# Kernel tuning notes

Hardware: AMD Instinct MI355X
Metric: run time of the kernel (lower is better)

Reference implementation:

```python
import jax, jax.numpy as jnp
import numpy as np

B, T, D = 2, 2048, 1024
N, H = 16, 64  # num_heads, head_dim
LOG2E = 1.442695041
NEG_INF = -1.0e9


def setup_inputs() -> dict:
    key = jax.random.key(0)
    ks = jax.random.split(key, 6)
    return {
        "input_tensor": jax.random.normal(ks[0], (B, T, D), dtype=jnp.float32),
        "attention_mask": jax.random.randint(ks[1], (B, 1, T, T), 0, 2, dtype=jnp.int32),
        "wq": jax.random.normal(ks[2], (D, N, H), dtype=jnp.float32),
        "bq": jnp.zeros((N, H), dtype=jnp.float32),
        "wk": jax.random.normal(ks[3], (D, N, H), dtype=jnp.float32),
        "bk": jnp.zeros((N, H), dtype=jnp.float32),
        "wv": jax.random.normal(ks[4], (D, N, H), dtype=jnp.float32),
        "bv": jnp.zeros((N, H), dtype=jnp.float32),
        "wo": jax.random.normal(ks[5], (D, N, H), dtype=jnp.float32),
        "bo": jnp.zeros((D,), dtype=jnp.float32),
        "per_dim_scale": jnp.zeros((H,), dtype=jnp.float32),
    }


def reference(input_tensor, attention_mask, wq, bq, wk, bk, wv, bv, wo, bo, per_dim_scale):
    # QKV projections: [B,T,D] x [D,N,H] -> [B,T,N,H]
    q = jnp.einsum('btd,dnh->btnh', input_tensor, wq) + bq
    k = jnp.einsum('btd,dnh->btnh', input_tensor, wk) + bk
    v = jnp.einsum('btd,dnh->btnh', input_tensor, wv) + bv
    # per-dim query scaling: (log2(e)/sqrt(H)) * softplus(per_dim_scale)
    scale = (LOG2E / jnp.sqrt(jnp.asarray(H, q.dtype))) * jax.nn.softplus(per_dim_scale)
    q = q * scale
    # scores: [B,N,T,S]
    scores = jnp.einsum('btnh,bsnh->bnts', q, k)
    scores = jnp.where(attention_mask == 0, jnp.asarray(NEG_INF, scores.dtype), scores)
    weights = jax.nn.softmax(scores, axis=-1)
    # AV: [B,N,T,S] x [B,S,N,H] -> [B,T,N,H]
    attn_out = jnp.einsum('bnts,bsnh->btnh', weights, v)
    # output projection: [B,T,N,H] x [D,N,H] -> [B,T,D]
    return jnp.einsum('btnh,dnh->btd', attn_out, wo) + bo
```

## Files before the change

### kernel.cpp

```cpp
#include <hip/hip_runtime.h>
#include <math.h>

typedef __bf16 bf16;
typedef __attribute__((ext_vector_type(8))) __bf16 bf16x8;
typedef __attribute__((ext_vector_type(4))) __bf16 bf16x4;
typedef __attribute__((ext_vector_type(4))) float f32x4;

#define BB 2
#define TT 2048
#define DD 1024
#define NHD 16
#define HD 64
#define MM (BB*TT)
#define LOG2E_F 1.442695041f
#define NEGINF_F (-1.0e9f)

__device__ __forceinline__ void gld16(const bf16* g, bf16* l)
{
    __builtin_amdgcn_global_load_lds(
        (const __attribute__((address_space(1))) unsigned int*)g,
        (__attribute__((address_space(3))) unsigned int*)l, 16, 0, 0);
}

__global__ __launch_bounds__(256)
void prep_all(const float* __restrict__ X, const int* __restrict__ m,
              const float* __restrict__ wq, const float* __restrict__ wk,
              const float* __restrict__ wv, const float* __restrict__ wo,
              bf16* __restrict__ Xh, bf16* __restrict__ Xl,
              bf16* __restrict__ qkh, bf16* __restrict__ qkl,
              bf16* __restrict__ vh, bf16* __restrict__ ob,
              unsigned* __restrict__ bits)
{
    __shared__ float tile[32][33];
    const int bid = blockIdx.x;
    const int t   = threadIdx.x;

    if (bid < 4096) {
        int i = bid * 256 + t;
        float4 v = ((const float4*)X)[i];
        float f[4] = {v.x, v.y, v.z, v.w};
        bf16x4 h, l;
        #pragma unroll
        for (int j = 0; j < 4; ++j) {
            bf16 hh = (bf16)f[j];
            h[j] = hh;
            l[j] = (bf16)(f[j] - (float)hh);
        }
        *(bf16x4*)(Xh + (size_t)i * 4) = h;
        *(bf16x4*)(Xl + (size_t)i * 4) = l;
        return;
    }
    if (bid < 8192) {
        const int idx = bid - 4096;
        const int z   = idx >> 10;
        const int bx  = (idx & 31) << 5;
        const int by  = ((idx >> 5) & 31) << 5;
        const int r   = t >> 3;
        const int c4  = (t & 7) << 2;
        if (z == 3) {
            float4 v = *(const float4*)(wo + (size_t)(by + r) * 1024 + bx + c4);
            bf16x4 o = { (bf16)v.x, (bf16)v.y, (bf16)v.z, (bf16)v.w };
            *(bf16x4*)(ob + (size_t)(by + r) * 1024 + bx + c4) = o;
            return;
        }
        const float* src = (z == 0) ? wq : ((z == 1) ? wk : wv);
        bf16* oh = (z == 0) ? qkh : ((z == 1) ? qkh + 1048576 : vh);
        bf16* ol = (z == 0) ? qkl : ((z == 1) ? qkl + 1048576 : nullptr);
        float4 v = *(const float4*)(src + (size_t)(by + r) * 1024 + bx + c4);
        tile[r][c4+0] = v.x; tile[r][c4+1] = v.y;
        tile[r][c4+2] = v.z; tile[r][c4+3] = v.w;
        __syncthreads();
        bf16x4 hv, lv;
        #pragma unroll
        for (int j = 0; j < 4; ++j) {
            float f = tile[c4 + j][r];
            bf16 h = (bf16)f;
            hv[j] = h;
            lv[j] = (bf16)(f - (float)h);
        }
        *(bf16x4*)(oh + (size_t)(bx + r) * 1024 + by + c4) = hv;
        if (ol)
            *(bf16x4*)(ol + (size_t)(bx + r) * 1024 + by + c4) = lv;
        return;
    }
    {
        int i = (bid - 8192) * 256 + t;
        int lane = t & 63;
        int v = m[i];
        unsigned long long bl = __ballot(v != 0);
        if ((lane & 31) == 0)
            bits[i >> 5] = (unsigned)(bl >> (lane & 32));
    }
}

__global__ __launch_bounds__(256)
void gemm_proj(const bf16* __restrict__ Xh, const bf16* __restrict__ Xl,
               const bf16* __restrict__ Wh, const bf16* __restrict__ Wl,
               const bf16* __restrict__ Wvh,
               const float* __restrict__ bq, const float* __restrict__ bk,
               const float* __restrict__ bv, const float* __restrict__ pds,
               bf16* __restrict__ oQh, bf16* __restrict__ oQl,
               bf16* __restrict__ oKh, bf16* __restrict__ oKl,
               bf16* __restrict__ oVt)
{
    __shared__ bf16 S[4][128 * 32];

    const int bid  = blockIdx.x;
    const int t    = threadIdx.x;
    const int lane = t & 63;
    const int w    = t >> 6;
    const int quad = lane >> 4, l15 = lane & 15;
    const int wm   = (w >> 1) << 6;
    const int wn   = (w & 1)  << 6;

    const int jr0 = ((w * 2 + 0) << 4) + (lane >> 2);
    const int jr1 = ((w * 2 + 1) << 4) + (lane >> 2);
    const int kch = (lane & 3) << 3;
    const int off0 = (w * 2 + 0) * 512;
    const int off1 = (w * 2 + 1) * 512;

    if (bid < 512) {
        const int m0 = (bid >> 4) << 7;
        const int n0 = (bid & 15) << 7;
        bf16* Ah = S[0]; bf16* Al = S[1]; bf16* Bh = S[2]; bf16* Bl = S[3];

        const bf16* pAh0 = Xh + (size_t)(m0 + jr0) * DD + kch;
        const bf16* pAh1 = Xh + (size_t)(m0 + jr1) * DD + kch;
        const bf16* pAl0 = Xl + (size_t)(m0 + jr0) * DD + kch;
        const bf16* pAl1 = Xl + (size_t)(m0 + jr1) * DD + kch;
        const bf16* pBh0 = Wh + (size_t)(n0 + jr0) * DD + kch;
        const bf16* pBh1 = Wh + (size_t)(n0 + jr1) * DD + kch;
        const bf16* pBl0 = Wl + (size_t)(n0 + jr0) * DD + kch;
        const bf16* pBl1 = Wl + (size_t)(n0 + jr1) * DD + kch;

        f32x4 acc[4][4] = {};

        for (int k0 = 0; k0 < DD; k0 += 32) {
            __syncthreads();
            gld16(pAh0 + k0, Ah + off0);  gld16(pAh1 + k0, Ah + off1);
            gld16(pAl0 + k0, Al + off0);  gld16(pAl1 + k0, Al + off1);
            gld16(pBh0 + k0, Bh + off0);  gld16(pBh1 + k0, Bh + off1);
            gld16(pBl0 + k0, Bl + off0);  gld16(pBl1 + k0, Bl + off1);
            __syncthreads();

            bf16x8 ah[4], bh[4];
            #pragma unroll
            for (int mt = 0; mt < 4; ++mt)
                ah[mt] = *(const bf16x8*)(Ah + (wm + (mt << 4) + l15) * 32 + (quad << 3));
            #pragma unroll
            for (int nt = 0; nt < 4; ++nt)
                bh[nt] = *(const bf16x8*)(Bh + (wn + (nt << 4) + l15) * 32 + (quad << 3));
            #pragma unroll
            for (int mt = 0; mt < 4; ++mt)
                #pragma unroll
                for (int nt = 0; nt < 4; ++nt)
                    acc[mt][nt] = __builtin_amdgcn_mfma_f32_16x16x32_bf16(
                        ah[mt], bh[nt], acc[mt][nt], 0, 0, 0);

            bf16x8 bl[4];
            #pragma unroll
            for (int nt = 0; nt < 4; ++nt)
                bl[nt] = *(const bf16x8*)(Bl + (wn + (nt << 4) + l15) * 32 + (quad << 3));
            #pragma unroll
            for (int mt = 0; mt < 4; ++mt)
                #pragma unroll
                for (int nt = 0; nt < 4; ++nt)
                    acc[mt][nt] = __builtin_amdgcn_mfma_f32_16x16x32_bf16(
                        ah[mt], bl[nt], acc[mt][nt], 0, 0, 0);

            bf16x8 al[4];
            #pragma unroll
            for (int mt = 0; mt < 4; ++mt)
                al[mt] = *(const bf16x8*)(Al + (wm + (mt << 4) + l15) * 32 + (quad << 3));
            #pragma unroll
            for (int mt = 0; mt < 4; ++mt)
                #pragma unroll
                for (int nt = 0; nt < 4; ++nt)
                    acc[mt][nt] = __builtin_amdgcn_mfma_f32_16x16x32_bf16(
                        al[mt], bh[nt], acc[mt][nt], 0, 0, 0);
        }

        #pragma unroll
        for (int nt = 0; nt < 4; ++nt) {
            const int col = n0 + wn + (nt << 4) + l15;
            const int isQ = (col < 1024);
            const int nh  = col & 1023;
            const int n   = nh >> 6, h = nh & 63;
            const float bcol = isQ ? bq[nh] : bk[nh];
            float s = 1.f;
            if (isQ) {
                float x  = pds[h];
                float sp = fmaxf(x, 0.f) + log1pf(expf(-fabsf(x)));
                s = (LOG2E_F * LOG2E_F / 8.0f) * sp;
            }
            bf16* dH = isQ ? oQh : oKh;
            bf16* dL = isQ ? oQl : oKl;
            #pragma unroll
            for (int mt = 0; mt < 4; ++mt) {
                #pragma unroll
                for (int reg = 0; reg < 4; ++reg) {
                    const int row = m0 + wm + (mt << 4) + (quad << 2) + reg;
                    const int bi  = row >> 11;
                    const int tt  = row & (TT - 1);
                    float val = (acc[mt][nt][reg] + bcol) * s;
                    const size_t idx = (((size_t)bi * NHD + n) * TT + tt) * HD + h;
                    bf16 hi = (bf16)val;
                    dH[idx] = hi;
                    dL[idx] = (bf16)(val - (float)hi);
                }
            }
        }
    } else {
        const int idx = bid - 512;
        const int m0  = (idx >> 5) << 7;
        const int n0  = (idx & 31) << 7;
        bf16* As = S[0]; bf16* Bs = S[2];

        const bf16* Ap0 = Wvh + (size_t)(m0 + jr0) * DD + kch;
        const bf16* Ap1 = Wvh + (size_t)(m0 + jr1) * DD + kch;
        const bf16* Bp0 = Xh  + (size_t)(n0 + jr0) * DD + kch;
        const bf16* Bp1 = Xh  + (size_t)(n0 + jr1) * DD + kch;

        f32x4 acc[4][4] = {};

        for (int k0 = 0; k0 < DD; k0 += 32) {
            __syncthreads();
            gld16(Ap0 + k0, As + off0);
            gld16(Ap1 + k0, As + off1);
            gld16(Bp0 + k0, Bs + off0);
            gld16(Bp1 + k0, Bs + off1);
            __syncthreads();
            bf16x8 af[4], bfm[4];
            #pragma unroll
            for (int mt = 0; mt < 4; ++mt)
                af[mt] = *(const bf16x8*)(As + (wm + (mt << 4) + l15) * 32 + (quad << 3));
            #pragma unroll
            for (int nt = 0; nt < 4; ++nt)
                bfm[nt] = *(const bf16x8*)(Bs + (wn + (nt << 4) + l15) * 32 + (quad << 3));
            #pragma unroll
            for (int mt = 0; mt < 4; ++mt)
                #pragma unroll
                for (int nt = 0; nt < 4; ++nt)
                    acc[mt][nt] = __builtin_amdgcn_mfma_f32_16x16x32_bf16(
                        af[mt], bfm[nt], acc[mt][nt], 0, 0, 0);
        }

        #pragma unroll
        for (int nt = 0; nt < 4; ++nt) {
            const int col = n0 + wn + (nt << 4) + l15;
            const int bi  = col >> 11;
            const int tt  = col & (TT - 1);
            #pragma unroll
            for (int mt = 0; mt < 4; ++mt) {
                #pragma unroll
                for (int reg = 0; reg < 4; ++reg) {
                    const int row = m0 + wm + (mt << 4) + (quad << 2) + reg;
                    float val = acc[mt][nt][reg] + bv[row];
                    oVt[((size_t)bi * 1024 + row) * TT + tt] = (bf16)val;
                }
            }
        }
    }
}

__global__ __launch_bounds__(256)
void gemm_out(const bf16* __restrict__ A, const bf16* __restrict__ Bt,
              const float* __restrict__ bias, float* __restrict__ oF)
{
    __shared__ bf16 As[128 * 32];
    __shared__ bf16 Bs[128 * 32];

    const int t    = threadIdx.x;
    const int lane = t & 63;
    const int w    = t >> 6;
    const int quad = lane >> 4, l15 = lane & 15;
    const int m0   = blockIdx.y << 7;
    const int n0   = blockIdx.x << 7;
    const int wm   = (w >> 1) << 6;
    const int wn   = (w & 1)  << 6;

    const int jr0 = ((w * 2 + 0) << 4) + (lane >> 2);
    const int jr1 = ((w * 2 + 1) << 4) + (lane >> 2);
    const int kch = (lane & 3) << 3;

    bf16* lA0 = As + (w * 2 + 0) * 512;
    bf16* lA1 = As + (w * 2 + 1) * 512;
    bf16* lB0 = Bs + (w * 2 + 0) * 512;
    bf16* lB1 = Bs + (w * 2 + 1) * 512;

    const bf16* Ap0 = A  + (size_t)(m0 + jr0) * DD + kch;
    const bf16* Ap1 = A  + (size_t)(m0 + jr1) * DD + kch;
    const bf16* Bp0 = Bt + (size_t)(n0 + jr0) * DD + kch;
    const bf16* Bp1 = Bt + (size_t)(n0 + jr1) * DD + kch;

    f32x4 acc[4][4] = {};

    for (int k0 = 0; k0 < DD; k0 += 32) {
        __syncthreads();
        gld16(Ap0 + k0, lA0);
        gld16(Ap1 + k0, lA1);
        gld16(Bp0 + k0, lB0);
        gld16(Bp1 + k0, lB1);
        __syncthreads();
        bf16x8 af[4], bfm[4];
        #pragma unroll
        for (int mt = 0; mt < 4; ++mt)
            af[mt] = *(const bf16x8*)(As + (wm + (mt << 4) + l15) * 32 + (quad << 3));
        #pragma unroll
        for (int nt = 0; nt < 4; ++nt)
            bfm[nt] = *(const bf16x8*)(Bs + (wn + (nt << 4) + l15) * 32 + (quad << 3));
        #pragma unroll
        for (int mt = 0; mt < 4; ++mt)
            #pragma unroll
            for (int nt = 0; nt < 4; ++nt)
                acc[mt][nt] = __builtin_amdgcn_mfma_f32_16x16x32_bf16(
                    af[mt], bfm[nt], acc[mt][nt], 0, 0, 0);
    }

    #pragma unroll
    for (int nt = 0; nt < 4; ++nt) {
        const int col = n0 + wn + (nt << 4) + l15;
        const float bcol = bias[col];
        #pragma unroll
        for (int mt = 0; mt < 4; ++mt) {
            #pragma unroll
            for (int reg = 0; reg < 4; ++reg) {
                const int row = m0 + wm + (mt << 4) + (quad << 2) + reg;
                oF[(size_t)row * DD + col] = acc[mt][nt][reg] + bcol;
            }
        }
    }
}

__global__ __launch_bounds__(512)
void attn_mfma(const bf16* __restrict__ Qh, const bf16* __restrict__ Ql,
               const bf16* __restrict__ Kh, const bf16* __restrict__ Kl,
               const bf16* __restrict__ Vt, const unsigned* __restrict__ mbits,
               bf16* __restrict__ AO)
{
    __shared__ bf16 Ksh[64][72];
    __shared__ bf16 Ksl[64][72];
    __shared__ bf16 Vts[64][72];
    __shared__ bf16 Ps[8][16][72];
    __shared__ unsigned msk[128][2];

    const int t    = threadIdx.x;
    const int lane = t & 63;
    const int w    = t >> 6;
    const int quad = lane >> 4, l15 = lane & 15;
    const int bn   = blockIdx.y;
    const int b    = bn >> 4, n = bn & 15;
    const int q0   = blockIdx.x << 7;

    const bf16* Qbh = Qh + (size_t)bn * TT * HD;
    const bf16* Qbl = Ql + (size_t)bn * TT * HD;
    const bf16* Kbh = Kh + (size_t)bn * TT * HD;
    const bf16* Kbl = Kl + (size_t)bn * TT * HD;
    const bf16* Vtb = Vt + (size_t)bn * HD * TT;

    const int qrow = q0 + (w << 4) + l15;
    bf16x8 qfh[2], qfl[2];
    qfh[0] = *(const bf16x8*)(Qbh + (size_t)qrow * HD + (quad << 3));
    qfh[1] = *(const bf16x8*)(Qbh + (size_t)qrow * HD + 32 + (quad << 3));
    qfl[0] = *(const bf16x8*)(Qbl + (size_t)qrow * HD + (quad << 3));
    qfl[1] = *(const bf16x8*)(Qbl + (size_t)qrow * HD + 32 + (quad << 3));

    f32x4 O[4];
    #pragma unroll
    for (int i = 0; i < 4; ++i) O[i] = (f32x4){0.f,0.f,0.f,0.f};
    float m_i = -INFINITY;
    float l_i = 0.f;

    const int rS = t >> 3, cS = (t & 7) << 3;

    for (int kb = 0; kb < TT; kb += 64) {
        bf16x8 khv = *(const bf16x8*)(Kbh + (size_t)(kb + rS) * HD + cS);
        bf16x8 klv = *(const bf16x8*)(Kbl + (size_t)(kb + rS) * HD + cS);
        bf16x8 vv  = *(const bf16x8*)(Vtb + (size_t)rS * TT + kb + cS);
        unsigned mw = 0;
        if (t < 256)
            mw = mbits[((size_t)b * TT + q0 + (t >> 1)) * (TT / 32) + (kb >> 5) + (t & 1)];

        __syncthreads();
        *(bf16x8*)&Ksh[rS][cS] = khv;
        *(bf16x8*)&Ksl[rS][cS] = klv;
        *(bf16x8*)&Vts[rS][cS] = vv;
        if (t < 256) msk[t >> 1][t & 1] = mw;
        __syncthreads();

        f32x4 s_acc[4];
        #pragma unroll
        for (int i = 0; i < 4; ++i) s_acc[i] = (f32x4){0.f,0.f,0.f,0.f};
        #pragma unroll
        for (int k2 = 0; k2 < 2; ++k2) {
            #pragma unroll
            for (int nt = 0; nt < 4; ++nt) {
                bf16x8 bkh = *(const bf16x8*)&Ksh[(nt << 4) + l15][(k2 << 5) + (quad << 3)];
                bf16x8 bkl = *(const bf16x8*)&Ksl[(nt << 4) + l15][(k2 << 5) + (quad << 3)];
                s_acc[nt] = __builtin_amdgcn_mfma_f32_16x16x32_bf16(bkh, qfh[k2], s_acc[nt], 0, 0, 0);
                s_acc[nt] = __builtin_amdgcn_mfma_f32_16x16x32_bf16(bkl, qfh[k2], s_acc[nt], 0, 0, 0);
                s_acc[nt] = __builtin_amdgcn_mfma_f32_16x16x32_bf16(bkh, qfl[k2], s_acc[nt], 0, 0, 0);
            }
        }

        const unsigned w0 = msk[(w << 4) + l15][0];
        const unsigned w1 = msk[(w << 4) + l15][1];
        float sv[16];
        #pragma unroll
        for (int nt = 0; nt < 4; ++nt) {
            const unsigned word = (nt & 2) ? w1 : w0;
            #pragma unroll
            for (int reg = 0; reg < 4; ++reg) {
                const int bit = ((nt & 1) << 4) + (quad << 2) + reg;
                sv[nt * 4 + reg] = ((word >> bit) & 1u) ? s_acc[nt][reg] : NEGINF_F;
            }
        }
        float mx = sv[0];
        #pragma unroll
        for (int i = 1; i < 16; ++i) mx = fmaxf(mx, sv[i]);
        mx = fmaxf(mx, __shfl_xor(mx, 16));
        mx = fmaxf(mx, __shfl_xor(mx, 32));
        const float mnew  = fmaxf(m_i, mx);
        const float alpha = exp2f(m_i - mnew);
        float p[16], sum = 0.f;
        #pragma unroll
        for (int i = 0; i < 16; ++i) { p[i] = exp2f(sv[i] - mnew); sum += p[i]; }
        sum += __shfl_xor(sum, 16);
        sum += __shfl_xor(sum, 32);
        l_i = l_i * alpha + sum;
        m_i = mnew;
        #pragma unroll
        for (int nt = 0; nt < 4; ++nt) {
            O[nt][0] *= alpha; O[nt][1] *= alpha;
            O[nt][2] *= alpha; O[nt][3] *= alpha;
            bf16x4 pv = { (bf16)p[nt * 4 + 0], (bf16)p[nt * 4 + 1],
                          (bf16)p[nt * 4 + 2], (bf16)p[nt * 4 + 3] };
            *(bf16x4*)&Ps[w][l15][(nt << 4) + (quad << 2)] = pv;
        }

        #pragma unroll
        for (int s2 = 0; s2 < 2; ++s2) {
            bf16x8 ap = *(const bf16x8*)&Ps[w][l15][(s2 << 5) + (quad << 3)];
            #pragma unroll
            for (int nt = 0; nt < 4; ++nt) {
                bf16x8 bv = *(const bf16x8*)&Vts[(nt << 4) + l15][(s2 << 5) + (quad << 3)];
                O[nt] = __builtin_amdgcn_mfma_f32_16x16x32_bf16(bv, ap, O[nt], 0, 0, 0);
            }
        }
    }

    {
        const float inv = 1.0f / l_i;
        const size_t base = ((size_t)b * TT + qrow) * (NHD * HD) + (size_t)n * HD;
        #pragma unroll
        for (int nt = 0; nt < 4; ++nt) {
            bf16x4 o = { (bf16)(O[nt][0] * inv), (bf16)(O[nt][1] * inv),
                         (bf16)(O[nt][2] * inv), (bf16)(O[nt][3] * inv) };
            *(bf16x4*)(AO + base + (nt << 4) + (quad << 2)) = o;
        }
    }
}

extern "C" void kernel_launch(void* const* d_in, const int* in_sizes, int n_in,
                              void* d_out, int out_size, void* d_ws, size_t ws_size,
                              hipStream_t stream)
{
    const float* X   = (const float*)d_in[0];
    const int*   msk = (const int*)d_in[1];
    const float* wq  = (const float*)d_in[2];
    const float* bq  = (const float*)d_in[3];
    const float* wk  = (const float*)d_in[4];
    const float* bk  = (const float*)d_in[5];
    const float* wv  = (const float*)d_in[6];
    const float* bv  = (const float*)d_in[7];
    const float* wo  = (const float*)d_in[8];
    const float* bo  = (const float*)d_in[9];
    const float* pds = (const float*)d_in[10];
    float* out = (float*)d_out;

    bf16* ws   = (bf16*)d_ws;
    bf16* Xh   = ws;
    bf16* Xl   = ws + 4194304;
    bf16* WQKh = ws + 8388608;
    bf16* WQKl = ws + 10485760;
    bf16* Wvh  = ws + 12582912;
    bf16* Wob  = ws + 13631488;
    bf16* Qhb  = ws + 14680064;
    bf16* Qlb  = ws + 18874368;
    bf16* Khb  = ws + 23068672;
    bf16* Klb  = ws + 27262976;
    unsigned* mbits = (unsigned*)(ws + 31457280);
    bf16* Vtb  = Xl;
    bf16* AOb  = Xh;

    dim3 blk(256);

    prep_all<<<40960, blk, 0, stream>>>(X, msk, wq, wk, wv, wo,
                                        Xh, Xl, WQKh, WQKl, Wvh, Wob, mbits);

    gemm_proj<<<768, blk, 0, stream>>>(
        Xh, Xl, WQKh, WQKl, Wvh, bq, bk, bv, pds,
        Qhb, Qlb, Khb, Klb, (bf16*)(ws + 32505856));

    dim3 ga(TT / 128, BB * NHD);
    attn_mfma<<<ga, dim3(512), 0, stream>>>(
        Qhb, Qlb, Khb, Klb, (bf16*)(ws + 32505856), mbits, AOb);

    gemm_out<<<dim3(8, 32), blk, 0, stream>>>(AOb, Wob, bo, out);
}
```

Before: 319.4 us.

## Vectorize mask bit-packing, use 64-bit mask words, narrow output GEMM tile

After: 309.3 us. 1.03x faster.

```diff
diff --git a/kernel.cpp b/kernel.cpp
--- a/kernel.cpp
+++ b/kernel.cpp
@@ -29,7 +29,7 @@
               bf16* __restrict__ Xh, bf16* __restrict__ Xl,
               bf16* __restrict__ qkh, bf16* __restrict__ qkl,
               bf16* __restrict__ vh, bf16* __restrict__ ob,
-              unsigned* __restrict__ bits)
+              unsigned char* __restrict__ bits)
 {
     __shared__ float tile[32][33];
     const int bid = blockIdx.x;
@@ -85,11 +85,14 @@
     }
     {
         int i = (bid - 8192) * 256 + t;
-        int lane = t & 63;
-        int v = m[i];
-        unsigned long long bl = __ballot(v != 0);
-        if ((lane & 31) == 0)
-            bits[i >> 5] = (unsigned)(bl >> (lane & 32));
+        const int4* mp = (const int4*)m + (size_t)i * 2;
+        int4 a  = mp[0];
+        int4 b4 = mp[1];
+        unsigned v = (a.x  != 0)       | ((a.y  != 0) << 1)
+                   | ((a.z  != 0) << 2) | ((a.w  != 0) << 3)
+                   | ((b4.x != 0) << 4) | ((b4.y != 0) << 5)
+                   | ((b4.z != 0) << 6) | ((b4.w != 0) << 7);
+        bits[i] = (unsigned char)v;
     }
 }
 
@@ -268,57 +271,55 @@
               const float* __restrict__ bias, float* __restrict__ oF)
 {
     __shared__ bf16 As[128 * 32];
-    __shared__ bf16 Bs[128 * 32];
+    __shared__ bf16 Bs[64 * 32];
 
     const int t    = threadIdx.x;
     const int lane = t & 63;
     const int w    = t >> 6;
     const int quad = lane >> 4, l15 = lane & 15;
     const int m0   = blockIdx.y << 7;
-    const int n0   = blockIdx.x << 7;
+    const int n0   = blockIdx.x << 6;
     const int wm   = (w >> 1) << 6;
-    const int wn   = (w & 1)  << 6;
+    const int wn   = (w & 1)  << 5;
 
     const int jr0 = ((w * 2 + 0) << 4) + (lane >> 2);
     const int jr1 = ((w * 2 + 1) << 4) + (lane >> 2);
+    const int jrB = (w << 4) + (lane >> 2);
     const int kch = (lane & 3) << 3;
 
     bf16* lA0 = As + (w * 2 + 0) * 512;
     bf16* lA1 = As + (w * 2 + 1) * 512;
-    bf16* lB0 = Bs + (w * 2 + 0) * 512;
-    bf16* lB1 = Bs + (w * 2 + 1) * 512;
+    bf16* lB  = Bs + w * 512;
 
     const bf16* Ap0 = A  + (size_t)(m0 + jr0) * DD + kch;
     const bf16* Ap1 = A  + (size_t)(m0 + jr1) * DD + kch;
-    const bf16* Bp0 = Bt + (size_t)(n0 + jr0) * DD + kch;
-    const bf16* Bp1 = Bt + (size_t)(n0 + jr1) * DD + kch;
-
-    f32x4 acc[4][4] = {};
+    const bf16* Bp  = Bt + (size_t)(n0 + jrB) * DD + kch;
+
+    f32x4 acc[4][2] = {};
 
     for (int k0 = 0; k0 < DD; k0 += 32) {
         __syncthreads();
         gld16(Ap0 + k0, lA0);
         gld16(Ap1 + k0, lA1);
-        gld16(Bp0 + k0, lB0);
-        gld16(Bp1 + k0, lB1);
+        gld16(Bp + k0, lB);
         __syncthreads();
-        bf16x8 af[4], bfm[4];
+        bf16x8 af[4], bfm[2];
         #pragma unroll
         for (int mt = 0; mt < 4; ++mt)
             af[mt] = *(const bf16x8*)(As + (wm + (mt << 4) + l15) * 32 + (quad << 3));
         #pragma unroll
-        for (int nt = 0; nt < 4; ++nt)
+        for (int nt = 0; nt < 2; ++nt)
             bfm[nt] = *(const bf16x8*)(Bs + (wn + (nt << 4) + l15) * 32 + (quad << 3));
         #pragma unroll
         for (int mt = 0; mt < 4; ++mt)
             #pragma unroll
-            for (int nt = 0; nt < 4; ++nt)
+            for (int nt = 0; nt < 2; ++nt)
                 acc[mt][nt] = __builtin_amdgcn_mfma_f32_16x16x32_bf16(
                     af[mt], bfm[nt], acc[mt][nt], 0, 0, 0);
     }
 
     #pragma unroll
-    for (int nt = 0; nt < 4; ++nt) {
+    for (int nt = 0; nt < 2; ++nt) {
         const int col = n0 + wn + (nt << 4) + l15;
         const float bcol = bias[col];
         #pragma unroll
@@ -335,14 +336,15 @@
 __global__ __launch_bounds__(512)
 void attn_mfma(const bf16* __restrict__ Qh, const bf16* __restrict__ Ql,
                const bf16* __restrict__ Kh, const bf16* __restrict__ Kl,
-               const bf16* __restrict__ Vt, const unsigned* __restrict__ mbits,
+               const bf16* __restrict__ Vt,
+               const unsigned long long* __restrict__ mb64,
                bf16* __restrict__ AO)
 {
     __shared__ bf16 Ksh[64][72];
     __shared__ bf16 Ksl[64][72];
     __shared__ bf16 Vts[64][72];
     __shared__ bf16 Ps[8][16][72];
-    __shared__ unsigned msk[128][2];
+    __shared__ unsigned long long msk64[128];
 
     const int t    = threadIdx.x;
     const int lane = t & 63;
@@ -371,21 +373,22 @@
     float m_i = -INFINITY;
     float l_i = 0.f;
 
-    const int rS = t >> 3, cS = (t & 7) << 3;
+    const int rS = t >> 3;
+    const int cS = (((t & 7) ^ (rS & 7)) << 3);
 
     for (int kb = 0; kb < TT; kb += 64) {
         bf16x8 khv = *(const bf16x8*)(Kbh + (size_t)(kb + rS) * HD + cS);
         bf16x8 klv = *(const bf16x8*)(Kbl + (size_t)(kb + rS) * HD + cS);
         bf16x8 vv  = *(const bf16x8*)(Vtb + (size_t)rS * TT + kb + cS);
-        unsigned mw = 0;
-        if (t < 256)
-            mw = mbits[((size_t)b * TT + q0 + (t >> 1)) * (TT / 32) + (kb >> 5) + (t & 1)];
+        unsigned long long mw = 0;
+        if (t < 128)
+            mw = mb64[((size_t)b * TT + q0 + t) * (TT / 64) + (kb >> 6)];
 
         __syncthreads();
         *(bf16x8*)&Ksh[rS][cS] = khv;
         *(bf16x8*)&Ksl[rS][cS] = klv;
         *(bf16x8*)&Vts[rS][cS] = vv;
-        if (t < 256) msk[t >> 1][t & 1] = mw;
+        if (t < 128) msk64[t] = mw;
         __syncthreads();
 
         f32x4 s_acc[4];
@@ -403,16 +406,17 @@
             }
         }
 
-        const unsigned w0 = msk[(w << 4) + l15][0];
-        const unsigned w1 = msk[(w << 4) + l15][1];
+        const unsigned long long word = msk64[(w << 4) + l15];
+        const unsigned w0 = (unsigned)word;
+        const unsigned w1 = (unsigned)(word >> 32);
         float sv[16];
         #pragma unroll
         for (int nt = 0; nt < 4; ++nt) {
-            const unsigned word = (nt & 2) ? w1 : w0;
+            const unsigned wrd = (nt & 2) ? w1 : w0;
             #pragma unroll
             for (int reg = 0; reg < 4; ++reg) {
                 const int bit = ((nt & 1) << 4) + (quad << 2) + reg;
-                sv[nt * 4 + reg] = ((word >> bit) & 1u) ? s_acc[nt][reg] : NEGINF_F;
+                sv[nt * 4 + reg] = ((wrd >> bit) & 1u) ? s_acc[nt][reg] : NEGINF_F;
             }
         }
         float mx = sv[0];
@@ -489,22 +493,22 @@
     bf16* Qlb  = ws + 18874368;
     bf16* Khb  = ws + 23068672;
     bf16* Klb  = ws + 27262976;
-    unsigned* mbits = (unsigned*)(ws + 31457280);
-    bf16* Vtb  = Xl;
+    unsigned char* mbits = (unsigned char*)(ws + 31457280);
+    bf16* Vtb  = ws + 32505856;
     bf16* AOb  = Xh;
 
     dim3 blk(256);
 
-    prep_all<<<40960, blk, 0, stream>>>(X, msk, wq, wk, wv, wo,
+    prep_all<<<12288, blk, 0, stream>>>(X, msk, wq, wk, wv, wo,
                                         Xh, Xl, WQKh, WQKl, Wvh, Wob, mbits);
 
     gemm_proj<<<768, blk, 0, stream>>>(
         Xh, Xl, WQKh, WQKl, Wvh, bq, bk, bv, pds,
-        Qhb, Qlb, Khb, Klb, (bf16*)(ws + 32505856));
+        Qhb, Qlb, Khb, Klb, Vtb);
 
     dim3 ga(TT / 128, BB * NHD);
     attn_mfma<<<ga, dim3(512), 0, stream>>>(
-        Qhb, Qlb, Khb, Klb, (bf16*)(ws + 32505856), mbits, AOb);
-
-    gemm_out<<<dim3(8, 32), blk, 0, stream>>>(AOb, Wob, bo, out);
+        Qhb, Qlb, Khb, Klb, Vtb, (const unsigned long long*)mbits, AOb);
+
+    gemm_out<<<dim3(16, 32), blk, 0, stream>>>(AOb, Wob, bo, out);
 }
```
